# Performance work log

Measured on AMD Instinct MI355X. Metric: run time of the kernel, lower is better.

Reference implementation:

```python
import jax, jax.numpy as jnp
import numpy as np

N = 8192
E = 131072
IN_DIM = 3000
HID = 512      # gcn1 out = HID // 2 = 256
OUT = 64
EPS = 1e-12


def gcn_conv(x, W, b, src, dst, n):
    """PyG GCNConv: add self-loops, symmetric norm, gather-matmul-scatter."""
    xw = x @ W                                   # [n, out]
    loop = jnp.arange(n, dtype=src.dtype)
    s = jnp.concatenate([src, loop])             # source j
    d = jnp.concatenate([dst, loop])             # target i
    deg = jax.ops.segment_sum(jnp.ones(s.shape[0], dtype=xw.dtype), d, num_segments=n)
    dinv = deg ** -0.5                           # deg >= 1 due to self-loops
    norm = dinv[s] * dinv[d]                     # [E+n]
    out = jax.ops.segment_sum(norm[:, None] * xw[s], d, num_segments=n)
    return out + b


def avg_readout(emb, mask):
    vsum = mask @ emb                            # [N, h]
    row_sum = jnp.sum(mask, axis=1, keepdims=True)
    g = vsum / row_sum
    nrm = jnp.maximum(jnp.linalg.norm(g, axis=1, keepdims=True), EPS)
    return g / nrm                               # F.normalize(p=2, dim=1)


def bilinear(h, c, Wd, bd):
    # nn.Bilinear(n_h, n_h, 1): out[n,o] = sum_ij h[n,i] Wd[o,i,j] c[n,j] + bd[o]
    return jnp.einsum('ni,oij,nj->no', h, Wd, c) + bd


def setup_inputs() -> dict:
    key = jax.random.key(0)
    k1, k2, k3, k4, k5, k6, k7 = jax.random.split(key, 7)
    gene_data = jax.random.normal(k1, (N, IN_DIM), dtype=jnp.float32)
    # sparse binary neighborhood mask (~16 neighbors/row) + self so row sums > 0
    mask = (jax.random.uniform(k2, (N, N)) < (16.0 / N)).astype(jnp.float32)
    mask = jnp.maximum(mask, jnp.eye(N, dtype=jnp.float32))
    spatial_edge_index = jax.random.randint(k3, (2, E), 0, N, dtype=jnp.int64)
    perm = jax.random.permutation(k4, N).astype(jnp.int64)
    h1 = HID // 2
    W1 = jax.random.normal(k5, (IN_DIM, h1), dtype=jnp.float32) / np.sqrt(IN_DIM)
    b1 = jnp.zeros((h1,), dtype=jnp.float32)
    W2 = jax.random.normal(k6, (h1, OUT), dtype=jnp.float32) / np.sqrt(h1)
    b2 = jnp.zeros((OUT,), dtype=jnp.float32)
    Wd = jax.random.normal(k7, (1, OUT, OUT), dtype=jnp.float32) / np.sqrt(OUT)
    bd = jnp.zeros((1,), dtype=jnp.float32)
    return {"gene_data": gene_data, "mask": mask, "W1": W1, "b1": b1,
            "W2": W2, "b2": b2, "Wd": Wd, "bd": bd,
            "spatial_edge_index": spatial_edge_index, "perm": perm}


def reference(gene_data, mask, W1, b1, W2, b2, Wd, bd, spatial_edge_index, perm):
    src, dst = spatial_edge_index[0], spatial_edge_index[1]
    n = gene_data.shape[0]
    x1 = gene_data
    x1_c = gene_data[perm]                       # permuted (corrupted) graph
    # dropout inactive (eval mode, p=0.0)
    x1 = jax.nn.relu(gcn_conv(x1, W1, b1, src, dst, n))
    x1_c = jax.nn.relu(gcn_conv(x1_c, W1, b1, src, dst, n))
    x1 = jax.nn.relu(gcn_conv(x1, W2, b2, src, dst, n))
    x1_c = jax.nn.relu(gcn_conv(x1_c, W2, b2, src, dst, n))
    g1 = jax.nn.sigmoid(avg_readout(x1, mask))
    g1_c = jax.nn.sigmoid(avg_readout(x1_c, mask))
    ret1 = jnp.concatenate([bilinear(x1, g1, Wd, bd), bilinear(x1_c, g1, Wd, bd)], axis=1)
    ret1_c = jnp.concatenate([bilinear(x1_c, g1_c, Wd, bd), bilinear(x1, g1_c, Wd, bd)], axis=1)
    return (x1, ret1, ret1_c)
```

## Files before the change

kernel.cpp:

```cpp
#include <hip/hip_runtime.h>
#include <hip/hip_bf16.h>

#define NN 8192
#define NMASK 8191
#define IND 3000
#define INDP 3008
#define H1 256
#define OUTD 64

typedef __bf16 bf16x8 __attribute__((ext_vector_type(8)));
typedef float floatx4 __attribute__((ext_vector_type(4)));

__device__ __forceinline__ unsigned short f2b(float f) {
    __hip_bfloat16 h = __float2bfloat16(f);
    unsigned short u;
    __builtin_memcpy(&u, &h, 2);
    return u;
}


__global__ void k_probe(float code, float* out) {
    if (threadIdx.x == 0 && blockIdx.x == 0) out[0] = code;
}


__global__ void k_detect2(const unsigned* __restrict__ a, const unsigned* __restrict__ b,
                          int pairs, int* __restrict__ flags) {
    const unsigned* r = (blockIdx.x == 0) ? a : b;
    __shared__ int cnt;
    if (threadIdx.x == 0) cnt = 0;
    __syncthreads();
    int z = 0;
    for (int k = threadIdx.x; k < pairs; k += blockDim.x)
        if (r[2 * k + 1] == 0u) z++;
    atomicAdd(&cnt, z);
    __syncthreads();
    if (threadIdx.x == 0) flags[blockIdx.x] = (cnt > pairs / 2) ? 1 : 0;
}


__global__ void k_prep(const unsigned* __restrict__ eraw, const unsigned* __restrict__ praw,
                       const int* __restrict__ flags, int* __restrict__ eidx32,
                       int* __restrict__ perm32, int* __restrict__ deg, int E, int n) {
    int i = blockIdx.x * blockDim.x + threadIdx.x;
    if (i < 2 * E) {
        unsigned v = flags[0] ? eraw[2 * (size_t)i] : eraw[i];
        int x = (int)(v & (unsigned)NMASK);
        eidx32[i] = x;
        if (i >= E) atomicAdd(&deg[x], 1);
    } else {
        int j = i - 2 * E;
        if (j < n) {
            unsigned v = flags[1] ? praw[2 * (size_t)j] : praw[j];
            perm32[j] = (int)(v & (unsigned)NMASK);
        }
    }
}


__global__ __launch_bounds__(1024) void k_scan(const int* __restrict__ deg,
                                               int* __restrict__ row_ptr,
                                               int* __restrict__ cursor,
                                               float* __restrict__ dinv, int n) {
    __shared__ int sums[1024];
    int t = threadIdx.x;
    int per = n / 1024;
    int base = t * per;
    int s = 0;
    for (int u = 0; u < per; ++u) s += deg[base + u];
    sums[t] = s;
    __syncthreads();
    for (int off = 1; off < 1024; off <<= 1) {
        int v = (t >= off) ? sums[t - off] : 0;
        __syncthreads();
        sums[t] += v;
        __syncthreads();
    }
    int run = (t == 0) ? 0 : sums[t - 1];
    for (int u = 0; u < per; ++u) {
        int i = base + u;
        row_ptr[i] = run;
        cursor[i] = run;
        int d = deg[i];
        dinv[i] = rsqrtf((float)(1 + d));
        run += d;
    }
    if (t == 1023) row_ptr[n] = run;
}

__global__ void k_scatter(const int* __restrict__ src, const int* __restrict__ dst,
                          int* __restrict__ cursor, int* __restrict__ col, int E) {
    int e = blockIdx.x * blockDim.x + threadIdx.x;
    if (e < E) {
        int d = dst[e];
        int p = atomicAdd(&cursor[d], 1);
        if (p >= 0 && p < E) col[p] = src[e];
    }
}

__global__ void k_transpose_f2b(const float* __restrict__ in,
                                __hip_bfloat16* __restrict__ out, int R, int C, int ld) {
    int idx = blockIdx.x * blockDim.x + threadIdx.x;
    if (idx < R * C) {
        int r = idx / C, c = idx % C;
        out[(size_t)c * ld + r] = __float2bfloat16(in[idx]);
    }
}


__global__ __launch_bounds__(256) void k_gemm1(const float* __restrict__ A,
                                               const __hip_bfloat16* __restrict__ Bt,
                                               float* __restrict__ C) {
    __shared__ __align__(16) unsigned short As[64 * 72];
    __shared__ __align__(16) unsigned short Bs[64 * 72];
    int t = threadIdx.x;
    int n0 = blockIdx.x * 64;
    int m0 = blockIdx.y * 64;
    int lane = t & 63;
    int w = t >> 6;
    int srow = t >> 2;
    int schunk = (t & 3) * 16;
    const float* Arow = A + (size_t)(m0 + srow) * IND + schunk;
    const unsigned short* Brow = (const unsigned short*)Bt + (size_t)(n0 + srow) * INDP + schunk;

    floatx4 acc0 = {0.f, 0.f, 0.f, 0.f}, acc1 = acc0, acc2 = acc0, acc3 = acc0;
    int msub = w * 16;
    int arow = msub + (lane & 15);
    int koff = (lane >> 4) * 8;
    int nlo = lane & 15;

    for (int k0 = 0; k0 < IND; k0 += 64) {
        uint4 av0 = make_uint4(0u, 0u, 0u, 0u), av1 = av0, bv0 = av0, bv1 = av0;
        {
            int kk = k0 + schunk;
            if (kk < IND) {
                const float* ap = Arow + k0;
                float4 f0 = *reinterpret_cast<const float4*>(ap);
                float4 f1 = *reinterpret_cast<const float4*>(ap + 4);
                unsigned short t8[8] = {f2b(f0.x), f2b(f0.y), f2b(f0.z), f2b(f0.w),
                                        f2b(f1.x), f2b(f1.y), f2b(f1.z), f2b(f1.w)};
                __builtin_memcpy(&av0, t8, 16);
                bv0 = *reinterpret_cast<const uint4*>(Brow + k0);
            }
            if (kk + 8 < IND) {
                const float* ap = Arow + k0 + 8;
                float4 f0 = *reinterpret_cast<const float4*>(ap);
                float4 f1 = *reinterpret_cast<const float4*>(ap + 4);
                unsigned short t8[8] = {f2b(f0.x), f2b(f0.y), f2b(f0.z), f2b(f0.w),
                                        f2b(f1.x), f2b(f1.y), f2b(f1.z), f2b(f1.w)};
                __builtin_memcpy(&av1, t8, 16);
                bv1 = *reinterpret_cast<const uint4*>(Brow + k0 + 8);
            }
        }
        __syncthreads();
        *reinterpret_cast<uint4*>(&As[srow * 72 + schunk]) = av0;
        *reinterpret_cast<uint4*>(&As[srow * 72 + schunk + 8]) = av1;
        *reinterpret_cast<uint4*>(&Bs[srow * 72 + schunk]) = bv0;
        *reinterpret_cast<uint4*>(&Bs[srow * 72 + schunk + 8]) = bv1;
        __syncthreads();
#pragma unroll
        for (int ks = 0; ks < 64; ks += 32) {
            bf16x8 af = *reinterpret_cast<const bf16x8*>(&As[arow * 72 + ks + koff]);
            bf16x8 b0 = *reinterpret_cast<const bf16x8*>(&Bs[(0 + nlo) * 72 + ks + koff]);
            bf16x8 b1 = *reinterpret_cast<const bf16x8*>(&Bs[(16 + nlo) * 72 + ks + koff]);
            bf16x8 b2 = *reinterpret_cast<const bf16x8*>(&Bs[(32 + nlo) * 72 + ks + koff]);
            bf16x8 b3 = *reinterpret_cast<const bf16x8*>(&Bs[(48 + nlo) * 72 + ks + koff]);
            acc0 = __builtin_amdgcn_mfma_f32_16x16x32_bf16(af, b0, acc0, 0, 0, 0);
            acc1 = __builtin_amdgcn_mfma_f32_16x16x32_bf16(af, b1, acc1, 0, 0, 0);
            acc2 = __builtin_amdgcn_mfma_f32_16x16x32_bf16(af, b2, acc2, 0, 0, 0);
            acc3 = __builtin_amdgcn_mfma_f32_16x16x32_bf16(af, b3, acc3, 0, 0, 0);
        }
    }
    int crow = msub + (lane >> 4) * 4;
    int ccol = lane & 15;
    floatx4 accs[4] = {acc0, acc1, acc2, acc3};
#pragma unroll
    for (int j = 0; j < 4; ++j) {
#pragma unroll
        for (int r = 0; r < 4; ++r) {
            C[(size_t)(m0 + crow + r) * H1 + (n0 + j * 16 + ccol)] = accs[j][r];
        }
    }
}


__global__ __launch_bounds__(256) void k_gemm2(const __hip_bfloat16* __restrict__ A,
                                               const __hip_bfloat16* __restrict__ Bt,
                                               float* __restrict__ C,
                                               int M, int N, int K) {
    __shared__ __align__(16) unsigned short As[64 * 40];
    __shared__ __align__(16) unsigned short Bs[64 * 40];
    int t = threadIdx.x;
    int m0 = blockIdx.x * 64;
    int n0 = blockIdx.y * 64;
    int lane = t & 63;
    int w = t >> 6;
    int srow = t >> 2;
    int schunk = (t & 3) * 8;
    size_t aoff = (size_t)(m0 + srow) * K + schunk;
    const unsigned short* Brow = (const unsigned short*)Bt + (size_t)(n0 + srow) * K + schunk;

    floatx4 acc0 = {0.f, 0.f, 0.f, 0.f}, acc1 = acc0, acc2 = acc0, acc3 = acc0;
    int msub = w * 16;
    int arow = msub + (lane & 15);
    int koff = (lane >> 4) * 8;
    int nlo = lane & 15;

    for (int k0 = 0; k0 < K; k0 += 32) {
        uint4 av = *reinterpret_cast<const uint4*>((const unsigned short*)A + aoff + k0);
        uint4 bv = *reinterpret_cast<const uint4*>(Brow + k0);
        __syncthreads();
        *reinterpret_cast<uint4*>(&As[srow * 40 + schunk]) = av;
        *reinterpret_cast<uint4*>(&Bs[srow * 40 + schunk]) = bv;
        __syncthreads();
        bf16x8 af = *reinterpret_cast<const bf16x8*>(&As[arow * 40 + koff]);
        bf16x8 bf0 = *reinterpret_cast<const bf16x8*>(&Bs[(0 + nlo) * 40 + koff]);
        bf16x8 bf1 = *reinterpret_cast<const bf16x8*>(&Bs[(16 + nlo) * 40 + koff]);
        bf16x8 bf2 = *reinterpret_cast<const bf16x8*>(&Bs[(32 + nlo) * 40 + koff]);
        bf16x8 bf3 = *reinterpret_cast<const bf16x8*>(&Bs[(48 + nlo) * 40 + koff]);
        acc0 = __builtin_amdgcn_mfma_f32_16x16x32_bf16(af, bf0, acc0, 0, 0, 0);
        acc1 = __builtin_amdgcn_mfma_f32_16x16x32_bf16(af, bf1, acc1, 0, 0, 0);
        acc2 = __builtin_amdgcn_mfma_f32_16x16x32_bf16(af, bf2, acc2, 0, 0, 0);
        acc3 = __builtin_amdgcn_mfma_f32_16x16x32_bf16(af, bf3, acc3, 0, 0, 0);
    }
    int crow = msub + (lane >> 4) * 4;
    int ccol = lane & 15;
    floatx4 accs[4] = {acc0, acc1, acc2, acc3};
#pragma unroll
    for (int j = 0; j < 4; ++j) {
#pragma unroll
        for (int r = 0; r < 4; ++r) {
            C[(size_t)(m0 + crow + r) * N + (n0 + j * 16 + ccol)] = accs[j][r];
        }
    }
}


__global__ __launch_bounds__(256) void k_agg1(const float* __restrict__ xw1,
                                              const int* __restrict__ row_ptr,
                                              const int* __restrict__ col,
                                              const float* __restrict__ dinv,
                                              const int* __restrict__ perm,
                                              const float* __restrict__ b1,
                                              __hip_bfloat16* __restrict__ h_all, int n) {
    __shared__ int colS[64];
    __shared__ int pcolS[64];
    __shared__ float wS[64];
    int i = blockIdx.x;
    int c = threadIdx.x;
    float di = dinv[i];
    int pi = perm[i];
    float sw = di * di;
    float acc = sw * xw1[(size_t)i * H1 + c];
    float accc = sw * xw1[(size_t)pi * H1 + c];
    int s = row_ptr[i], e = row_ptr[i + 1];
    for (int base = s; base < e; base += 64) {
        int cnt = min(64, e - base);
        __syncthreads();
        if (c < cnt) {
            int j = col[base + c];
            colS[c] = j;
            wS[c] = di * dinv[j];
            pcolS[c] = perm[j];
        }
        __syncthreads();
#pragma unroll 4
        for (int u = 0; u < cnt; ++u) {
            float wv = wS[u];
            acc += wv * xw1[(size_t)colS[u] * H1 + c];
            accc += wv * xw1[(size_t)pcolS[u] * H1 + c];
        }
    }
    float b = b1[c];
    h_all[(size_t)i * H1 + c] = __float2bfloat16(fmaxf(acc + b, 0.f));
    h_all[(size_t)(n + i) * H1 + c] = __float2bfloat16(fmaxf(accc + b, 0.f));
}


__global__ __launch_bounds__(256) void k_agg2(const float* __restrict__ hw_all,
                                              const int* __restrict__ row_ptr,
                                              const int* __restrict__ col,
                                              const float* __restrict__ dinv,
                                              const float* __restrict__ b2,
                                              float* __restrict__ x1_all,
                                              float* __restrict__ out_x1, int n) {
    int lane = threadIdx.x & 63;
    int i = blockIdx.x * 4 + (threadIdx.x >> 6);
    float di = dinv[i];
    float sw = di * di;
    float acc = sw * hw_all[(size_t)i * OUTD + lane];
    float accc = sw * hw_all[(size_t)(n + i) * OUTD + lane];
    int s = row_ptr[i], e = row_ptr[i + 1];
#pragma unroll 4
    for (int t = s; t < e; ++t) {
        int j = col[t];
        float wv = di * dinv[j];
        acc += wv * hw_all[(size_t)j * OUTD + lane];
        accc += wv * hw_all[(size_t)(n + j) * OUTD + lane];
    }
    float b = b2[lane];
    float v = fmaxf(acc + b, 0.f);
    float vc = fmaxf(accc + b, 0.f);
    x1_all[(size_t)i * OUTD + lane] = v;
    x1_all[(size_t)(n + i) * OUTD + lane] = vc;
    out_x1[(size_t)i * OUTD + lane] = v;
}


__global__ __launch_bounds__(256) void k_readout(const float* __restrict__ mask,
                                                 const float* __restrict__ x1_all,
                                                 const float* __restrict__ Wd,
                                                 const float* __restrict__ bd,
                                                 float* __restrict__ ret1,
                                                 float* __restrict__ ret1c, int n) {
    int i = blockIdx.x;
    int lane = threadIdx.x & 63;
    int w = threadIdx.x >> 6;
    float acc = 0.f, accc = 0.f, rs = 0.f;
    const float* mrow = mask + (size_t)i * n;
    int quarter = n >> 2;
    int qbase = w * quarter;
    int iters = quarter / 256;
    for (int it = 0; it < iters; ++it) {
        int jb = qbase + it * 256 + lane * 4;
        floatx4 q = __builtin_nontemporal_load(reinterpret_cast<const floatx4*>(mrow + jb));
        bool nz = (q[0] != 0.f) || (q[1] != 0.f) || (q[2] != 0.f) || (q[3] != 0.f);
        unsigned long long bal = __ballot(nz);
        while (bal) {
            int l = __builtin_ctzll(bal);
            bal &= bal - 1;
            float s0 = __shfl(q[0], l), s1 = __shfl(q[1], l);
            float s2 = __shfl(q[2], l), s3 = __shfl(q[3], l);
            int j0 = qbase + it * 256 + l * 4;
            float sv[4] = {s0, s1, s2, s3};
#pragma unroll
            for (int u = 0; u < 4; ++u) {
                if (sv[u] != 0.f) {
                    float m = sv[u];
                    int j = j0 + u;
                    acc += m * x1_all[(size_t)j * OUTD + lane];
                    accc += m * x1_all[(size_t)(n + j) * OUTD + lane];
                    rs += m;
                }
            }
        }
    }
    __shared__ float sa[4][64], sc[4][64], sr[4];
    sa[w][lane] = acc;
    sc[w][lane] = accc;
    if (lane == 0) sr[w] = rs;
    __syncthreads();
    if (w == 0) {
        float tot = sa[0][lane] + sa[1][lane] + sa[2][lane] + sa[3][lane];
        float totc = sc[0][lane] + sc[1][lane] + sc[2][lane] + sc[3][lane];
        float rst = fmaxf(sr[0] + sr[1] + sr[2] + sr[3], 1e-20f);
        float g = tot / rst;
        float gc = totc / rst;
        float s1 = g * g, s2 = gc * gc;
#pragma unroll
        for (int off = 32; off; off >>= 1) {
            s1 += __shfl_xor(s1, off);
            s2 += __shfl_xor(s2, off);
        }
        float gn = g / fmaxf(sqrtf(s1), 1e-12f);
        float gnc = gc / fmaxf(sqrtf(s2), 1e-12f);
        float gsig = 1.f / (1.f + __expf(-gn));
        float gcsig = 1.f / (1.f + __expf(-gnc));
        float tg = 0.f, tgc = 0.f;
        const float* wrow = Wd + lane * 64;
#pragma unroll 8
        for (int j = 0; j < 64; ++j) {
            float gj = __shfl(gsig, j);
            float gcj = __shfl(gcsig, j);
            float wv = wrow[j];
            tg += wv * gj;
            tgc += wv * gcj;
        }
        float x = x1_all[(size_t)i * OUTD + lane];
        float xc = x1_all[(size_t)(n + i) * OUTD + lane];
        float r0 = x * tg, r1 = xc * tg, r2 = xc * tgc, r3 = x * tgc;
#pragma unroll
        for (int off = 32; off; off >>= 1) {
            r0 += __shfl_down(r0, off);
            r1 += __shfl_down(r1, off);
            r2 += __shfl_down(r2, off);
            r3 += __shfl_down(r3, off);
        }
        if (lane == 0) {
            float b = bd[0];
            ret1[(size_t)i * 2 + 0] = r0 + b;
            ret1[(size_t)i * 2 + 1] = r1 + b;
            ret1c[(size_t)i * 2 + 0] = r2 + b;
            ret1c[(size_t)i * 2 + 1] = r3 + b;
        }
    }
}


extern "C" void kernel_launch(void* const* d_in, const int* in_sizes, int n_in,
                              void* d_out, int out_size, void* d_ws, size_t ws_size,
                              hipStream_t stream) {
    const float* gene = (const float*)d_in[0];
    const float* mask = (const float*)d_in[1];
    const float* W1 = (const float*)d_in[2];
    const float* b1 = (const float*)d_in[3];
    const float* W2 = (const float*)d_in[4];
    const float* b2 = (const float*)d_in[5];
    const float* Wd = (const float*)d_in[6];
    const float* bd = (const float*)d_in[7];
    const unsigned* eidx_raw = (const unsigned*)d_in[8];
    const unsigned* perm_raw = (const unsigned*)d_in[9];
    const int n = NN;
    const int E = in_sizes[8] / 2;

    char* base = (char*)d_ws;
    char* p = base;
    auto alloc = [&](size_t bytes) -> char* {
        char* r = p;
        p += (bytes + 255) & ~(size_t)255;
        return r;
    };
    int* flags = (int*)alloc(256);
    int* eidx32 = (int*)alloc((size_t)2 * E * 4);
    int* perm32 = (int*)alloc((size_t)n * 4);
    int* deg = (int*)alloc((size_t)n * 4);
    int* row_ptr = (int*)alloc((size_t)(n + 1) * 4);
    int* cursor = (int*)alloc((size_t)n * 4);
    float* dinv = (float*)alloc((size_t)n * 4);
    int* col = (int*)alloc((size_t)E * 4);
    __hip_bfloat16* W2t = (__hip_bfloat16*)alloc((size_t)H1 * OUTD * 2);
    __hip_bfloat16* W1t = (__hip_bfloat16*)alloc((size_t)INDP * H1 * 2);
    float* xw1 = (float*)alloc((size_t)n * H1 * 4);
    __hip_bfloat16* h_all = (__hip_bfloat16*)alloc((size_t)2 * n * H1 * 2);
    size_t need = (size_t)(p - base);
    float* hw_all = xw1;
    float* x1_all = xw1 + (size_t)2 * n * OUTD;

    float* out_x1 = (float*)d_out;
    float* out_ret1 = out_x1 + (size_t)n * OUTD;
    float* out_ret1c = out_ret1 + (size_t)n * 2;

    if (ws_size < need) {
        k_probe<<<1, 64, 0, stream>>>(1000.f + (float)(ws_size >> 20), out_x1);
        return;
    }

    hipMemsetAsync(deg, 0, (size_t)n * 4, stream);

    k_detect2<<<2, 256, 0, stream>>>(eidx_raw, perm_raw, 2048, flags);
    k_prep<<<(2 * E + n + 255) / 256, 256, 0, stream>>>(eidx_raw, perm_raw, flags,
                                                        eidx32, perm32, deg, E, n);
    const int* srcv = eidx32;
    const int* dstv = eidx32 + E;

    k_scan<<<1, 1024, 0, stream>>>(deg, row_ptr, cursor, dinv, n);
    k_scatter<<<(E + 255) / 256, 256, 0, stream>>>(srcv, dstv, cursor, col, E);

    k_transpose_f2b<<<(IND * H1 + 255) / 256, 256, 0, stream>>>(W1, W1t, IND, H1, INDP);
    k_transpose_f2b<<<(H1 * OUTD + 255) / 256, 256, 0, stream>>>(W2, W2t, H1, OUTD, H1);

    k_gemm1<<<dim3(H1 / 64, n / 64), 256, 0, stream>>>(gene, W1t, xw1);

    k_agg1<<<n, H1, 0, stream>>>(xw1, row_ptr, col, dinv, perm32, b1, h_all, n);

    k_gemm2<<<dim3(2 * n / 64, OUTD / 64), 256, 0, stream>>>(h_all, W2t, hw_all, 2 * n, OUTD, H1);

    k_agg2<<<n / 4, 256, 0, stream>>>(hw_all, row_ptr, col, dinv, b2, x1_all, out_x1, n);

    k_readout<<<n, 256, 0, stream>>>(mask, x1_all, Wd, bd, out_ret1, out_ret1c, n);
}
```

Measured before the change: 606.2 us.

## Fuse setup kernels, prefetch GEMM tiles, vectorize aggregation and readout scan

Merges the memset, format detection, W1/W2 transposes and W1 pad zeroing into one launch, which saves several kernel launches. Both GEMMs now load the next K tile into registers before the MFMAs on the current tile, so global loads overlap with compute at the cost of more live registers. k_agg1 switches from a block per node with shared-memory staging to one wavefront per node doing float4 loads, with no __syncthreads. The readout mask scan reads 8 floats per lane per step, which halves the number of ballot iterations.

```diff
diff --git a/kernel.cpp b/kernel.cpp
--- a/kernel.cpp
+++ b/kernel.cpp
@@ -24,18 +24,48 @@
 }
 
 
-__global__ void k_detect2(const unsigned* __restrict__ a, const unsigned* __restrict__ b,
-                          int pairs, int* __restrict__ flags) {
-    const unsigned* r = (blockIdx.x == 0) ? a : b;
-    __shared__ int cnt;
-    if (threadIdx.x == 0) cnt = 0;
-    __syncthreads();
-    int z = 0;
-    for (int k = threadIdx.x; k < pairs; k += blockDim.x)
-        if (r[2 * k + 1] == 0u) z++;
-    atomicAdd(&cnt, z);
-    __syncthreads();
-    if (threadIdx.x == 0) flags[blockIdx.x] = (cnt > pairs / 2) ? 1 : 0;
+__global__ void k_pre(const unsigned* __restrict__ eraw, const unsigned* __restrict__ praw,
+                      int* __restrict__ flags, int* __restrict__ deg,
+                      const float* __restrict__ W1, const float* __restrict__ W2,
+                      __hip_bfloat16* __restrict__ W1t, __hip_bfloat16* __restrict__ W2t) {
+    int b = blockIdx.x;
+    int t = threadIdx.x;
+    if (b < 2) {
+        const unsigned* r = (b == 0) ? eraw : praw;
+        __shared__ int cnt;
+        if (t == 0) cnt = 0;
+        __syncthreads();
+        int z = 0;
+        for (int k = t; k < 2048; k += 256)
+            if (r[2 * k + 1] == 0u) z++;
+        atomicAdd(&cnt, z);
+        __syncthreads();
+        if (t == 0) flags[b] = (cnt > 1024) ? 1 : 0;
+    } else if (b < 10) {
+#pragma unroll
+        for (int u = 0; u < 4; ++u) deg[(b - 2) * 1024 + u * 256 + t] = 0;
+    } else if (b < 12) {
+        int idx = (b - 10) * 256 + t;
+#pragma unroll
+        for (int u = 0; u < 4; ++u) {
+            int k = idx * 4 + u;
+            int c = k >> 3;
+            int r = 3000 + (k & 7);
+            W1t[(size_t)c * INDP + r] = __float2bfloat16(0.f);
+        }
+    } else {
+        int idx = (b - 12) * 256 + t;
+        if (idx < IND * H1) {
+            int r = idx / H1, c = idx % H1;
+            W1t[(size_t)c * INDP + r] = __float2bfloat16(W1[idx]);
+        } else {
+            int j = idx - IND * H1;
+            if (j < H1 * OUTD) {
+                int r = j / OUTD, c = j % OUTD;
+                W2t[(size_t)c * H1 + r] = __float2bfloat16(W2[j]);
+            }
+        }
+    }
 }
 
 
@@ -98,15 +128,6 @@
     }
 }
 
-__global__ void k_transpose_f2b(const float* __restrict__ in,
-                                __hip_bfloat16* __restrict__ out, int R, int C, int ld) {
-    int idx = blockIdx.x * blockDim.x + threadIdx.x;
-    if (idx < R * C) {
-        int r = idx / C, c = idx % C;
-        out[(size_t)c * ld + r] = __float2bfloat16(in[idx]);
-    }
-}
-
 
 __global__ __launch_bounds__(256) void k_gemm1(const float* __restrict__ A,
                                                const __hip_bfloat16* __restrict__ Bt,
@@ -129,28 +150,38 @@
     int koff = (lane >> 4) * 8;
     int nlo = lane & 15;
 
+    float4 pa0, pa1, pa2, pa3;
+    uint4 pb0, pb1;
+    auto load_tile = [&](int k0) {
+        float4 z4 = make_float4(0.f, 0.f, 0.f, 0.f);
+        uint4 zu = make_uint4(0u, 0u, 0u, 0u);
+        pa0 = z4; pa1 = z4; pa2 = z4; pa3 = z4; pb0 = zu; pb1 = zu;
+        int kk = k0 + schunk;
+        if (kk < IND) {
+            const float* ap = Arow + k0;
+            pa0 = *reinterpret_cast<const float4*>(ap);
+            pa1 = *reinterpret_cast<const float4*>(ap + 4);
+            pb0 = *reinterpret_cast<const uint4*>(Brow + k0);
+        }
+        if (kk + 8 < IND) {
+            const float* ap = Arow + k0 + 8;
+            pa2 = *reinterpret_cast<const float4*>(ap);
+            pa3 = *reinterpret_cast<const float4*>(ap + 4);
+            pb1 = *reinterpret_cast<const uint4*>(Brow + k0 + 8);
+        }
+    };
+    load_tile(0);
     for (int k0 = 0; k0 < IND; k0 += 64) {
-        uint4 av0 = make_uint4(0u, 0u, 0u, 0u), av1 = av0, bv0 = av0, bv1 = av0;
+        uint4 av0, av1, bv0 = pb0, bv1 = pb1;
         {
-            int kk = k0 + schunk;
-            if (kk < IND) {
-                const float* ap = Arow + k0;
-                float4 f0 = *reinterpret_cast<const float4*>(ap);
-                float4 f1 = *reinterpret_cast<const float4*>(ap + 4);
-                unsigned short t8[8] = {f2b(f0.x), f2b(f0.y), f2b(f0.z), f2b(f0.w),
-                                        f2b(f1.x), f2b(f1.y), f2b(f1.z), f2b(f1.w)};
-                __builtin_memcpy(&av0, t8, 16);
-                bv0 = *reinterpret_cast<const uint4*>(Brow + k0);
-            }
-            if (kk + 8 < IND) {
-                const float* ap = Arow + k0 + 8;
-                float4 f0 = *reinterpret_cast<const float4*>(ap);
-                float4 f1 = *reinterpret_cast<const float4*>(ap + 4);
-                unsigned short t8[8] = {f2b(f0.x), f2b(f0.y), f2b(f0.z), f2b(f0.w),
-                                        f2b(f1.x), f2b(f1.y), f2b(f1.z), f2b(f1.w)};
-                __builtin_memcpy(&av1, t8, 16);
-                bv1 = *reinterpret_cast<const uint4*>(Brow + k0 + 8);
-            }
+            unsigned short t8[8] = {f2b(pa0.x), f2b(pa0.y), f2b(pa0.z), f2b(pa0.w),
+                                    f2b(pa1.x), f2b(pa1.y), f2b(pa1.z), f2b(pa1.w)};
+            __builtin_memcpy(&av0, t8, 16);
+        }
+        {
+            unsigned short t8[8] = {f2b(pa2.x), f2b(pa2.y), f2b(pa2.z), f2b(pa2.w),
+                                    f2b(pa3.x), f2b(pa3.y), f2b(pa3.z), f2b(pa3.w)};
+            __builtin_memcpy(&av1, t8, 16);
         }
         __syncthreads();
         *reinterpret_cast<uint4*>(&As[srow * 72 + schunk]) = av0;
@@ -158,6 +189,7 @@
         *reinterpret_cast<uint4*>(&Bs[srow * 72 + schunk]) = bv0;
         *reinterpret_cast<uint4*>(&Bs[srow * 72 + schunk + 8]) = bv1;
         __syncthreads();
+        if (k0 + 64 < IND) load_tile(k0 + 64);
 #pragma unroll
         for (int ks = 0; ks < 64; ks += 32) {
             bf16x8 af = *reinterpret_cast<const bf16x8*>(&As[arow * 72 + ks + koff]);
@@ -206,13 +238,18 @@
     int koff = (lane >> 4) * 8;
     int nlo = lane & 15;
 
+    uint4 pa = *reinterpret_cast<const uint4*>((const unsigned short*)A + aoff);
+    uint4 pb = *reinterpret_cast<const uint4*>(Brow);
     for (int k0 = 0; k0 < K; k0 += 32) {
-        uint4 av = *reinterpret_cast<const uint4*>((const unsigned short*)A + aoff + k0);
-        uint4 bv = *reinterpret_cast<const uint4*>(Brow + k0);
+        uint4 av = pa, bv = pb;
         __syncthreads();
         *reinterpret_cast<uint4*>(&As[srow * 40 + schunk]) = av;
         *reinterpret_cast<uint4*>(&Bs[srow * 40 + schunk]) = bv;
         __syncthreads();
+        if (k0 + 32 < K) {
+            pa = *reinterpret_cast<const uint4*>((const unsigned short*)A + aoff + k0 + 32);
+            pb = *reinterpret_cast<const uint4*>(Brow + k0 + 32);
+        }
         bf16x8 af = *reinterpret_cast<const bf16x8*>(&As[arow * 40 + koff]);
         bf16x8 bf0 = *reinterpret_cast<const bf16x8*>(&Bs[(0 + nlo) * 40 + koff]);
         bf16x8 bf1 = *reinterpret_cast<const bf16x8*>(&Bs[(16 + nlo) * 40 + koff]);
@@ -243,37 +280,35 @@
                                               const int* __restrict__ perm,
                                               const float* __restrict__ b1,
                                               __hip_bfloat16* __restrict__ h_all, int n) {
-    __shared__ int colS[64];
-    __shared__ int pcolS[64];
-    __shared__ float wS[64];
-    int i = blockIdx.x;
-    int c = threadIdx.x;
+    int lane = threadIdx.x & 63;
+    int i = blockIdx.x * 4 + (threadIdx.x >> 6);
     float di = dinv[i];
     int pi = perm[i];
     float sw = di * di;
-    float acc = sw * xw1[(size_t)i * H1 + c];
-    float accc = sw * xw1[(size_t)pi * H1 + c];
+    int c4 = lane * 4;
+    floatx4 acc = sw * *reinterpret_cast<const floatx4*>(xw1 + (size_t)i * H1 + c4);
+    floatx4 accc = sw * *reinterpret_cast<const floatx4*>(xw1 + (size_t)pi * H1 + c4);
     int s = row_ptr[i], e = row_ptr[i + 1];
-    for (int base = s; base < e; base += 64) {
-        int cnt = min(64, e - base);
-        __syncthreads();
-        if (c < cnt) {
-            int j = col[base + c];
-            colS[c] = j;
-            wS[c] = di * dinv[j];
-            pcolS[c] = perm[j];
-        }
-        __syncthreads();
 #pragma unroll 4
-        for (int u = 0; u < cnt; ++u) {
-            float wv = wS[u];
-            acc += wv * xw1[(size_t)colS[u] * H1 + c];
-            accc += wv * xw1[(size_t)pcolS[u] * H1 + c];
-        }
-    }
-    float b = b1[c];
-    h_all[(size_t)i * H1 + c] = __float2bfloat16(fmaxf(acc + b, 0.f));
-    h_all[(size_t)(n + i) * H1 + c] = __float2bfloat16(fmaxf(accc + b, 0.f));
+    for (int t = s; t < e; ++t) {
+        int j = col[t];
+        float wv = di * dinv[j];
+        int pj = perm[j];
+        acc += wv * *reinterpret_cast<const floatx4*>(xw1 + (size_t)j * H1 + c4);
+        accc += wv * *reinterpret_cast<const floatx4*>(xw1 + (size_t)pj * H1 + c4);
+    }
+    floatx4 b4 = *reinterpret_cast<const floatx4*>(b1 + c4);
+    ushort4 h0, h1;
+    h0.x = f2b(fmaxf(acc[0] + b4[0], 0.f));
+    h0.y = f2b(fmaxf(acc[1] + b4[1], 0.f));
+    h0.z = f2b(fmaxf(acc[2] + b4[2], 0.f));
+    h0.w = f2b(fmaxf(acc[3] + b4[3], 0.f));
+    h1.x = f2b(fmaxf(accc[0] + b4[0], 0.f));
+    h1.y = f2b(fmaxf(accc[1] + b4[1], 0.f));
+    h1.z = f2b(fmaxf(accc[2] + b4[2], 0.f));
+    h1.w = f2b(fmaxf(accc[3] + b4[3], 0.f));
+    *reinterpret_cast<ushort4*>(h_all + (size_t)i * H1 + c4) = h0;
+    *reinterpret_cast<ushort4*>(h_all + (size_t)(n + i) * H1 + c4) = h1;
 }
 
 
@@ -320,23 +355,23 @@
     const float* mrow = mask + (size_t)i * n;
     int quarter = n >> 2;
     int qbase = w * quarter;
-    int iters = quarter / 256;
-    for (int it = 0; it < iters; ++it) {
-        int jb = qbase + it * 256 + lane * 4;
-        floatx4 q = __builtin_nontemporal_load(reinterpret_cast<const floatx4*>(mrow + jb));
-        bool nz = (q[0] != 0.f) || (q[1] != 0.f) || (q[2] != 0.f) || (q[3] != 0.f);
+    for (int it = 0; it < 4; ++it) {
+        int jb = qbase + it * 512 + lane * 8;
+        floatx4 q0 = __builtin_nontemporal_load(reinterpret_cast<const floatx4*>(mrow + jb));
+        floatx4 q1 = __builtin_nontemporal_load(reinterpret_cast<const floatx4*>(mrow + jb + 4));
+        float qa[8] = {q0[0], q0[1], q0[2], q0[3], q1[0], q1[1], q1[2], q1[3]};
+        bool nz = false;
+#pragma unroll
+        for (int u = 0; u < 8; ++u) nz |= (qa[u] != 0.f);
         unsigned long long bal = __ballot(nz);
         while (bal) {
             int l = __builtin_ctzll(bal);
             bal &= bal - 1;
-            float s0 = __shfl(q[0], l), s1 = __shfl(q[1], l);
-            float s2 = __shfl(q[2], l), s3 = __shfl(q[3], l);
-            int j0 = qbase + it * 256 + l * 4;
-            float sv[4] = {s0, s1, s2, s3};
-#pragma unroll
-            for (int u = 0; u < 4; ++u) {
-                if (sv[u] != 0.f) {
-                    float m = sv[u];
+            int j0 = qbase + it * 512 + l * 8;
+#pragma unroll
+            for (int u = 0; u < 8; ++u) {
+                float m = __shfl(qa[u], l);
+                if (m != 0.f) {
                     int j = j0 + u;
                     acc += m * x1_all[(size_t)j * OUTD + lane];
                     accc += m * x1_all[(size_t)(n + j) * OUTD + lane];
@@ -445,9 +480,8 @@
         return;
     }
 
-    hipMemsetAsync(deg, 0, (size_t)n * 4, stream);
-
-    k_detect2<<<2, 256, 0, stream>>>(eidx_raw, perm_raw, 2048, flags);
+    k_pre<<<3076, 256, 0, stream>>>(eidx_raw, perm_raw, flags, deg, W1, W2, W1t, W2t);
+
     k_prep<<<(2 * E + n + 255) / 256, 256, 0, stream>>>(eidx_raw, perm_raw, flags,
                                                         eidx32, perm32, deg, E, n);
     const int* srcv = eidx32;
@@ -456,12 +490,9 @@
     k_scan<<<1, 1024, 0, stream>>>(deg, row_ptr, cursor, dinv, n);
     k_scatter<<<(E + 255) / 256, 256, 0, stream>>>(srcv, dstv, cursor, col, E);
 
-    k_transpose_f2b<<<(IND * H1 + 255) / 256, 256, 0, stream>>>(W1, W1t, IND, H1, INDP);
-    k_transpose_f2b<<<(H1 * OUTD + 255) / 256, 256, 0, stream>>>(W2, W2t, H1, OUTD, H1);
-
     k_gemm1<<<dim3(H1 / 64, n / 64), 256, 0, stream>>>(gene, W1t, xw1);
 
-    k_agg1<<<n, H1, 0, stream>>>(xw1, row_ptr, col, dinv, perm32, b1, h_all, n);
+    k_agg1<<<n / 4, 256, 0, stream>>>(xw1, row_ptr, col, dinv, perm32, b1, h_all, n);
 
     k_gemm2<<<dim3(2 * n / 64, OUTD / 64), 256, 0, stream>>>(h_all, W2t, hw_all, 2 * n, OUTD, H1);
 
```

Result: no change. 609.2 us (+0.5%).
